# Kernel optimization log

Hardware: AMD Instinct MI355X
Metric: run time of the kernel (lower is better)

Reference implementation:

```python
import jax, jax.numpy as jnp
import numpy as np

N_STEPS = 20
ALPHA, BETA = 0.9, 0.8  # synaptic / membrane decay (unused given zero carried state, kept for clarity)


def _lcn_spiking_layer(h, knn, w, b):
    """h: [N, d_in]; knn: [d_out, K] indices into d_in; w: [d_out, K]; b: [1, d_out].
    Gather K neighbors per output node, weight, reduce, then snntorch Synaptic
    update with zero carried state (the source never stores returned syn/mem):
      syn = ALPHA*0 + I = I ; reset = (prev_mem > thr) = 0 ; mem = BETA*0 + syn - 0 = I
    and the layer output is mem (the source keeps the 3rd return value)."""
    g = h[:, knn]                                  # [N, d_out, K] irregular gather
    cur = jnp.sum(g * w[None, :, :], axis=2) + b   # [N, d_out]
    syn = ALPHA * jnp.zeros_like(cur) + cur
    mem = BETA * jnp.zeros_like(cur) + syn         # reset term is zero
    return mem


def setup_inputs() -> dict:
    key = jax.random.key(0)
    B, T, IN_DIM, K, OUT = 32, N_STEPS, 14400, 25, 2
    dims = [7200, 3600, 1800, 900, 450]
    ks = jax.random.split(key, 13)
    inp = {"x": jax.random.normal(ks[0], (B, T, IN_DIM), dtype=jnp.float32)}
    prev = IN_DIM
    for i, d in enumerate(dims):
        inp[f"w{i}"] = jax.random.normal(ks[1 + i], (d, K), dtype=jnp.float32) * (2.0 / K) ** 0.5
        inp[f"b{i}"] = jnp.zeros((1, d), dtype=jnp.float32)
        inp[f"knn{i}"] = jax.random.randint(ks[6 + i], (d, K), 0, prev)
        prev = d
    inp["Wfc"] = jax.random.normal(ks[11], (dims[-1], OUT), dtype=jnp.float32) * (1.0 / dims[-1]) ** 0.5
    inp["bfc"] = jnp.zeros((OUT,), dtype=jnp.float32)
    return inp


def reference(x, w0, w1, w2, w3, w4, b0, b1, b2, b3, b4, Wfc, bfc,
              knn0, knn1, knn2, knn3, knn4):
    # Source loops over 20 timesteps with independent (state never carried) work;
    # fold time into batch to vectorize, then keep the last step's angle only,
    # exactly matching the returned value of the torch forward.
    B, T, D = x.shape
    h = x.reshape(B * T, D)
    layers = ((w0, b0, knn0), (w1, b1, knn1), (w2, b2, knn2), (w3, b3, knn3), (w4, b4, knn4))
    for w, b, knn in layers:
        h = _lcn_spiking_layer(h, knn, w, b)
    angle = h @ Wfc + bfc                     # [B*T, out_dim]
    angle = angle.reshape(B, T, -1)[:, -1]    # last timestep, as in the source
    return angle
```

## Files before the change

kernel.cpp:

```cpp
#include <hip/hip_runtime.h>
#include <hip/hip_bf16.h>


#define ROWS 32
#define TSTEPS 20
#define D0 14400
#define D1 7200
#define D2 3600
#define D3 1800
#define D4 900
#define D5 450
#define KNB 25

__global__ __launch_bounds__(256)
void lcn_layer_k(const float* __restrict__ hin_base, long long row_stride,
                 float* __restrict__ hout, int dout,
                 const float* __restrict__ w, const float* __restrict__ bvec,
                 const int* __restrict__ knn)
{
    const int j = blockIdx.x * blockDim.x + threadIdx.x;
    const int row = blockIdx.y;
    if (j >= dout) return;
    const float* hin = hin_base + (long long)row * row_stride;
    const int*   kn  = knn + j * KNB;
    const float* ww  = w   + j * KNB;
    float acc = bvec[j];
#pragma unroll
    for (int k = 0; k < KNB; ++k)
        acc += hin[kn[k]] * ww[k];
    hout[row * dout + j] = acc;
}

__global__ __launch_bounds__(1024)
void lcn_tail(const float* __restrict__ h3,
              const float* __restrict__ w3, const float* __restrict__ b3, const int* __restrict__ knn3,
              const float* __restrict__ w4, const float* __restrict__ b4, const int* __restrict__ knn4,
              const float* __restrict__ Wfc, const float* __restrict__ bfc,
              float* __restrict__ out)
{
    __shared__ float s3[D3];
    __shared__ float s4[D4];
    __shared__ float s5[D5];

    const int row = blockIdx.x;
    const float* hrow = h3 + row * D3;

    for (int i = threadIdx.x; i < D3; i += blockDim.x)
        s3[i] = hrow[i];
    __syncthreads();

    for (int j = threadIdx.x; j < D4; j += blockDim.x) {
        const int*   kn = knn3 + j * KNB;
        const float* ww = w3   + j * KNB;
        float acc = b3[j];
#pragma unroll
        for (int k = 0; k < KNB; ++k)
            acc += s3[kn[k]] * ww[k];
        s4[j] = acc;
    }
    __syncthreads();

    for (int j = threadIdx.x; j < D5; j += blockDim.x) {
        const int*   kn = knn4 + j * KNB;
        const float* ww = w4   + j * KNB;
        float acc = b4[j];
#pragma unroll
        for (int k = 0; k < KNB; ++k)
            acc += s4[kn[k]] * ww[k];
        s5[j] = acc;
    }
    __syncthreads();

    const int lane = threadIdx.x & 63;
    const int wid  = threadIdx.x >> 6;
    if (wid < 2) {
        float p = 0.0f;
        for (int i = lane; i < D5; i += 64)
            p += s5[i] * Wfc[i * 2 + wid];
#pragma unroll
        for (int off = 32; off; off >>= 1)
            p += __shfl_down(p, off, 64);
        if (lane == 0)
            out[row * 2 + wid] = p + bfc[wid];
    }
}

extern "C" void kernel_launch(void* const* d_in, const int* in_sizes, int n_in,
                              void* d_out, int out_size, void* d_ws, size_t ws_size,
                              hipStream_t stream)
{
    const float* x    = (const float*)d_in[0];
    const float* w0   = (const float*)d_in[1];
    const float* b0   = (const float*)d_in[2];
    const int*   knn0 = (const int*)  d_in[3];
    const float* w1   = (const float*)d_in[4];
    const float* b1   = (const float*)d_in[5];
    const int*   knn1 = (const int*)  d_in[6];
    const float* w2   = (const float*)d_in[7];
    const float* b2   = (const float*)d_in[8];
    const int*   knn2 = (const int*)  d_in[9];
    const float* w3   = (const float*)d_in[10];
    const float* b3   = (const float*)d_in[11];
    const int*   knn3 = (const int*)  d_in[12];
    const float* w4   = (const float*)d_in[13];
    const float* b4   = (const float*)d_in[14];
    const int*   knn4 = (const int*)  d_in[15];
    const float* Wfc  = (const float*)d_in[16];
    const float* bfc  = (const float*)d_in[17];
    float* out = (float*)d_out;

    float* h1 = (float*)d_ws;
    float* h2 = h1 + ROWS * D1;
    float* h3 = h2 + ROWS * D2;

    lcn_layer_k<<<dim3((D1 + 255) / 256, ROWS), dim3(256), 0, stream>>>(
        x + (size_t)(TSTEPS - 1) * D0, (long long)TSTEPS * D0, h1, D1, w0, b0, knn0);

    lcn_layer_k<<<dim3((D2 + 255) / 256, ROWS), dim3(256), 0, stream>>>(
        h1, D1, h2, D2, w1, b1, knn1);

    lcn_layer_k<<<dim3((D3 + 255) / 256, ROWS), dim3(256), 0, stream>>>(
        h2, D2, h3, D3, w2, b2, knn2);

    lcn_tail<<<dim3(ROWS), dim3(1024), 0, stream>>>(
        h3, w3, b3, knn3, w4, b4, knn4, Wfc, bfc, out);
}
```

Before: 146.4 us.

## Stage input rows in LDS for gather layers and split tail into more blocks

Each layer kernel now copies the full input row into shared memory with float4 loads, and each block then computes a fixed chunk of outputs using gathers from LDS instead of scattered global reads. Layer 3 is moved out of the single-block-per-row tail into its own multi-block launch, and the tail now handles only layer 4 and the FC with 256 threads. The aim is to replace random global gathers with LDS gathers and to raise parallelism in the tail. The cost is that every block re-reads its entire input row (up to 57.6 KB of LDS for layer 0), so global traffic is duplicated across blocks and occupancy is limited by LDS, and there is one extra launch.

```diff
diff --git a/kernel.cpp b/kernel.cpp
--- a/kernel.cpp
+++ b/kernel.cpp
@@ -12,55 +12,53 @@
 #define D5 450
 #define KNB 25
 
+template <int DIN, int DOUT, int JPB>
 __global__ __launch_bounds__(256)
-void lcn_layer_k(const float* __restrict__ hin_base, long long row_stride,
-                 float* __restrict__ hout, int dout,
-                 const float* __restrict__ w, const float* __restrict__ bvec,
-                 const int* __restrict__ knn)
+void layer_lds(const float* __restrict__ hin_base, long long row_stride,
+               float* __restrict__ hout,
+               const float* __restrict__ w, const float* __restrict__ bvec,
+               const int* __restrict__ knn)
 {
-    const int j = blockIdx.x * blockDim.x + threadIdx.x;
+    __shared__ float s[DIN];
     const int row = blockIdx.y;
-    if (j >= dout) return;
     const float* hin = hin_base + (long long)row * row_stride;
-    const int*   kn  = knn + j * KNB;
-    const float* ww  = w   + j * KNB;
-    float acc = bvec[j];
+
+    const float4* src = reinterpret_cast<const float4*>(hin);
+    float4* dst = reinterpret_cast<float4*>(s);
+#pragma unroll 1
+    for (int i = threadIdx.x; i < DIN / 4; i += 256)
+        dst[i] = src[i];
+    __syncthreads();
+
+    const int j0 = blockIdx.x * JPB;
+#pragma unroll 1
+    for (int j = j0 + threadIdx.x; j < j0 + JPB; j += 256) {
+        const int*   kn = knn + j * KNB;
+        const float* ww = w   + j * KNB;
+        float acc = bvec[j];
 #pragma unroll
-    for (int k = 0; k < KNB; ++k)
-        acc += hin[kn[k]] * ww[k];
-    hout[row * dout + j] = acc;
+        for (int k = 0; k < KNB; ++k)
+            acc += s[kn[k]] * ww[k];
+        hout[row * DOUT + j] = acc;
+    }
 }
 
-__global__ __launch_bounds__(1024)
-void lcn_tail(const float* __restrict__ h3,
-              const float* __restrict__ w3, const float* __restrict__ b3, const int* __restrict__ knn3,
-              const float* __restrict__ w4, const float* __restrict__ b4, const int* __restrict__ knn4,
-              const float* __restrict__ Wfc, const float* __restrict__ bfc,
-              float* __restrict__ out)
+__global__ __launch_bounds__(256)
+void lcn_l4_fc(const float* __restrict__ h4,
+               const float* __restrict__ w4, const float* __restrict__ b4, const int* __restrict__ knn4,
+               const float* __restrict__ Wfc, const float* __restrict__ bfc,
+               float* __restrict__ out)
 {
-    __shared__ float s3[D3];
     __shared__ float s4[D4];
     __shared__ float s5[D5];
 
     const int row = blockIdx.x;
-    const float* hrow = h3 + row * D3;
-
-    for (int i = threadIdx.x; i < D3; i += blockDim.x)
-        s3[i] = hrow[i];
+    const float* hrow = h4 + row * D4;
+    for (int i = threadIdx.x; i < D4; i += 256)
+        s4[i] = hrow[i];
     __syncthreads();
 
-    for (int j = threadIdx.x; j < D4; j += blockDim.x) {
-        const int*   kn = knn3 + j * KNB;
-        const float* ww = w3   + j * KNB;
-        float acc = b3[j];
-#pragma unroll
-        for (int k = 0; k < KNB; ++k)
-            acc += s3[kn[k]] * ww[k];
-        s4[j] = acc;
-    }
-    __syncthreads();
-
-    for (int j = threadIdx.x; j < D5; j += blockDim.x) {
+    for (int j = threadIdx.x; j < D5; j += 256) {
         const int*   kn = knn4 + j * KNB;
         const float* ww = w4   + j * KNB;
         float acc = b4[j];
@@ -112,16 +110,20 @@
     float* h1 = (float*)d_ws;
     float* h2 = h1 + ROWS * D1;
     float* h3 = h2 + ROWS * D2;
+    float* h4 = h3 + ROWS * D3;
 
-    lcn_layer_k<<<dim3((D1 + 255) / 256, ROWS), dim3(256), 0, stream>>>(
-        x + (size_t)(TSTEPS - 1) * D0, (long long)TSTEPS * D0, h1, D1, w0, b0, knn0);
+    layer_lds<D0, D1, 900><<<dim3(D1 / 900, ROWS), dim3(256), 0, stream>>>(
+        x + (size_t)(TSTEPS - 1) * D0, (long long)TSTEPS * D0, h1, w0, b0, knn0);
 
-    lcn_layer_k<<<dim3((D2 + 255) / 256, ROWS), dim3(256), 0, stream>>>(
-        h1, D1, h2, D2, w1, b1, knn1);
+    layer_lds<D1, D2, 450><<<dim3(D2 / 450, ROWS), dim3(256), 0, stream>>>(
+        h1, D1, h2, w1, b1, knn1);
 
-    lcn_layer_k<<<dim3((D3 + 255) / 256, ROWS), dim3(256), 0, stream>>>(
-        h2, D2, h3, D3, w2, b2, knn2);
+    layer_lds<D2, D3, 450><<<dim3(D3 / 450, ROWS), dim3(256), 0, stream>>>(
+        h2, D2, h3, w2, b2, knn2);
 
-    lcn_tail<<<dim3(ROWS), dim3(1024), 0, stream>>>(
-        h3, w3, b3, knn3, w4, b4, knn4, Wfc, bfc, out);
+    layer_lds<D3, D4, 225><<<dim3(D4 / 225, ROWS), dim3(256), 0, stream>>>(
+        h3, D3, h4, w3, b3, knn3);
+
+    lcn_l4_fc<<<dim3(ROWS), dim3(256), 0, stream>>>(
+        h4, w4, b4, knn4, Wfc, bfc, out);
 }
```

Measured after the change: 132.2 us. 9.7% less time.
